# Kernel optimization log

Measured on AMD Instinct MI355X. Metric: run time of the kernel, lower is better.

The kernel has to match this reference:

```python
import jax, jax.numpy as jnp
import numpy as np

N = 100000      # nodes
E = 1600000     # edges (avg degree 16)
F_IN = 256      # num_features
H2 = 128        # nhid * 2 (layer 1 width)
H = 64          # nhid (layer 2 width)
C = 10          # num_classes


def setup_inputs() -> dict:
    key = jax.random.key(0)
    ks = jax.random.split(key, 8)
    x = jax.random.normal(ks[0], (N, F_IN), dtype=jnp.float32)
    edge_index = jax.random.randint(ks[1], (2, E), 0, N, dtype=jnp.int64)
    W1 = jax.random.normal(ks[2], (F_IN, H2), dtype=jnp.float32) / np.float32(np.sqrt(F_IN))
    b1 = jnp.zeros((H2,), jnp.float32)
    W2 = jax.random.normal(ks[3], (H2, H), dtype=jnp.float32) / np.float32(np.sqrt(H2))
    b2 = jnp.zeros((H,), jnp.float32)
    Wl = jax.random.normal(ks[4], (H, C), dtype=jnp.float32) / np.float32(np.sqrt(H))
    bl = jnp.zeros((C,), jnp.float32)
    return {"x": x, "edge_index": edge_index, "W1": W1, "b1": b1,
            "W2": W2, "b2": b2, "Wl": Wl, "bl": bl}


def reference(x, edge_index, W1, b1, W2, b2, Wl, bl):
    # --- GCN normalization with self-loops (PyG GCNConv default) ---
    loops = jnp.arange(N, dtype=edge_index.dtype)
    src = jnp.concatenate([edge_index[0], loops])  # message sources
    dst = jnp.concatenate([edge_index[1], loops])  # message targets
    deg = jax.ops.segment_sum(jnp.ones(src.shape[0], x.dtype), dst, num_segments=N)
    dinv = jnp.where(deg > 0, jax.lax.rsqrt(deg), 0.0)
    norm = dinv[src] * dinv[dst]                   # [E+N]

    def gcn_conv(h, W, b):
        m = h @ W                                  # transform first (out_channels small)
        agg = jax.ops.segment_sum(m[src] * norm[:, None], dst, num_segments=N)
        return agg + b

    h = jax.nn.relu(gcn_conv(x, W1, b1))           # [N, H2]
    h = jax.nn.relu(gcn_conv(h, W2, b2))           # [N, H]
    logits = h @ Wl + bl                            # [N, C]
    return jax.nn.log_softmax(logits, axis=-1)
```

## Files before the change

### kernel.cpp

```cpp
#include <hip/hip_runtime.h>


typedef unsigned short ushort_t;
typedef unsigned int uint_t;
typedef __attribute__((ext_vector_type(8))) short short8;
typedef __attribute__((ext_vector_type(4))) float floatx4;

static __device__ __forceinline__ ushort_t f2bf(float f) {
    union { float f; uint_t u; } c; c.f = f;
    return (ushort_t)((c.u + 0x8000u) >> 16);
}
static __device__ __forceinline__ float bf2f(ushort_t h) {
    union { uint_t u; float f; } c; c.u = ((uint_t)h) << 16;
    return c.f;
}
static __device__ __forceinline__ float2 up2(uint_t p) {
    union { uint_t u; float f; } lo, hi;
    lo.u = p << 16; hi.u = p & 0xffff0000u;
    return make_float2(lo.f, hi.f);
}
static __device__ __forceinline__ void ld_lds16(void* lds, const void* g) {
    __builtin_amdgcn_global_load_lds(
        (const __attribute__((address_space(1))) unsigned int*)g,
        (__attribute__((address_space(3))) unsigned int*)lds, 16, 0, 0);
}


__global__ __launch_bounds__(256) void deg_pos_kernel(
    const int* __restrict__ dst, int* __restrict__ cnt, int* __restrict__ pos, int E) {
    int i4 = (blockIdx.x * 256 + threadIdx.x) * 4;
    if (i4 + 3 < E) {
        int4 d = *(const int4*)(dst + i4);
        int4 p;
        p.x = atomicAdd(&cnt[d.x], 1);
        p.y = atomicAdd(&cnt[d.y], 1);
        p.z = atomicAdd(&cnt[d.z], 1);
        p.w = atomicAdd(&cnt[d.w], 1);
        *(int4*)(pos + i4) = p;
    } else {
        for (int e = i4; e < E; e++)
            pos[e] = atomicAdd(&cnt[dst[e]], 1);
    }
}

__global__ void scan_block(const int* __restrict__ cnt, int* __restrict__ rowptr,
                           int* __restrict__ bsums, float* __restrict__ dinv, int n) {
    __shared__ int s[256];
    int i = blockIdx.x * 256 + threadIdx.x;
    int v = (i < n) ? cnt[i] : 0;
    if (i < n) dinv[i] = rsqrtf((float)(v + 1));
    s[threadIdx.x] = v;
    __syncthreads();
    for (int off = 1; off < 256; off <<= 1) {
        int t = (threadIdx.x >= off) ? s[threadIdx.x - off] : 0;
        __syncthreads();
        s[threadIdx.x] += t;
        __syncthreads();
    }
    if (i < n) rowptr[i] = s[threadIdx.x] - v;
    if (threadIdx.x == 255) bsums[blockIdx.x] = s[255];
}

__global__ void scan_tops(const int* __restrict__ bsums, int* __restrict__ boffs, int nb) {
    __shared__ int s[512];
    int v = (threadIdx.x < nb) ? bsums[threadIdx.x] : 0;
    s[threadIdx.x] = v;
    __syncthreads();
    for (int off = 1; off < 512; off <<= 1) {
        int t = (threadIdx.x >= off) ? s[threadIdx.x - off] : 0;
        __syncthreads();
        s[threadIdx.x] += t;
        __syncthreads();
    }
    if (threadIdx.x < nb) boffs[threadIdx.x] = s[threadIdx.x] - v;
}

__global__ void finalize_rowptr(int* __restrict__ rowptr, const int* __restrict__ boffs,
                                int n, int E) {
    int i = blockIdx.x * 256 + threadIdx.x;
    if (i < n) rowptr[i] += boffs[blockIdx.x];
    if (i == 0) rowptr[n] = E;
}

__global__ __launch_bounds__(256) void place_kernel(
    const int* __restrict__ src, const int* __restrict__ dst,
    const int* __restrict__ pos, const int* __restrict__ rowptr,
    int* __restrict__ csr, int E) {
    int i4 = (blockIdx.x * 256 + threadIdx.x) * 4;
    if (i4 + 3 < E) {
        int4 s = *(const int4*)(src + i4);
        int4 d = *(const int4*)(dst + i4);
        int4 p = *(const int4*)(pos + i4);
        csr[rowptr[d.x] + p.x] = s.x;
        csr[rowptr[d.y] + p.y] = s.y;
        csr[rowptr[d.z] + p.z] = s.z;
        csr[rowptr[d.w] + p.w] = s.w;
    } else {
        for (int e = i4; e < E; e++)
            csr[rowptr[dst[e]] + pos[e]] = src[e];
    }
}

__global__ void wcvt2_kernel(const float* __restrict__ W1, const float* __restrict__ W2,
                             ushort_t* __restrict__ W1t, ushort_t* __restrict__ W2t) {
    int i = blockIdx.x * 256 + threadIdx.x;
    if (i < 256 * 128) {
        int k = i / 128, n = i % 128;
        W1t[n * 256 + k] = f2bf(W1[i]);
    }
    int j = i - 256 * 128;
    if (j >= 0 && j < 128 * 64) {
        int k = j / 64, n = j % 64;
        W2t[n * 128 + k] = f2bf(W2[j]);
    }
}

__global__ __launch_bounds__(256) void gemm1_mfma(
    const float* __restrict__ A, const ushort_t* __restrict__ Bt,
    const float* __restrict__ dinv, ushort_t* __restrict__ out, int M) {
    __shared__ float    As[2][128 * 32];
    __shared__ ushort_t Bs[2][128 * 32];
    const int tid = threadIdx.x;
    const int l = tid & 63;
    const int wave = tid >> 6;
    const int wm = wave >> 1, wn = wave & 1;
    const int lrow = l & 15, hh = l >> 4;
    const int m0 = blockIdx.x * 128;

    int aslot0[4], aslot1[4], bslot[4];
    #pragma unroll
    for (int mt = 0; mt < 4; mt++) {
        int r = wm * 64 + mt * 16 + lrow;
        int sw = r & 7;
        aslot0[mt] = (r * 8 + ((2 * hh) ^ sw)) * 4;
        aslot1[mt] = (r * 8 + ((2 * hh + 1) ^ sw)) * 4;
    }
    #pragma unroll
    for (int nt = 0; nt < 4; nt++) {
        int nc = wn * 64 + nt * 16 + lrow;
        bslot[nt] = (nc * 4 + (hh ^ ((nc >> 2) & 3))) * 8;
    }

    floatx4 acc[4][4];
    #pragma unroll
    for (int mt = 0; mt < 4; mt++)
        #pragma unroll
        for (int nt = 0; nt < 4; nt++)
            acc[mt][nt] = (floatx4){0.f, 0.f, 0.f, 0.f};

    auto stage = [&](int buf, int k0) {
        #pragma unroll
        for (int i = 0; i < 4; i++) {
            int s = i * 256 + tid;
            int r = s >> 3, cp = s & 7;
            int cg = cp ^ (r & 7);
            int row = m0 + r; if (row >= M) row = M - 1;
            ld_lds16(&As[buf][s * 4], A + (size_t)row * 256 + k0 + cg * 4);
        }
        #pragma unroll
        for (int i = 0; i < 2; i++) {
            int s = i * 256 + tid;
            int nn = s >> 2, cp = s & 3;
            int cg = cp ^ ((nn >> 2) & 3);
            ld_lds16(&Bs[buf][s * 8], Bt + (size_t)nn * 256 + k0 + cg * 8);
        }
    };

    stage(0, 0);
    __syncthreads();
    int buf = 0;
    for (int kk = 0; kk < 8; kk++) {
        if (kk < 7) stage(buf ^ 1, (kk + 1) * 32);
        short8 afr[4], bfr[4];
        #pragma unroll
        for (int mt = 0; mt < 4; mt++) {
            float4 u = *(const float4*)&As[buf][aslot0[mt]];
            float4 v = *(const float4*)&As[buf][aslot1[mt]];
            short8 t;
            t[0] = (short)f2bf(u.x); t[1] = (short)f2bf(u.y);
            t[2] = (short)f2bf(u.z); t[3] = (short)f2bf(u.w);
            t[4] = (short)f2bf(v.x); t[5] = (short)f2bf(v.y);
            t[6] = (short)f2bf(v.z); t[7] = (short)f2bf(v.w);
            afr[mt] = t;
        }
        #pragma unroll
        for (int nt = 0; nt < 4; nt++)
            bfr[nt] = *(const short8*)&Bs[buf][bslot[nt]];
        #pragma unroll
        for (int mt = 0; mt < 4; mt++)
            #pragma unroll
            for (int nt = 0; nt < 4; nt++)
                acc[mt][nt] = __builtin_amdgcn_mfma_f32_16x16x32_bf16(
                    afr[mt], bfr[nt], acc[mt][nt], 0, 0, 0);
        __syncthreads();
        buf ^= 1;
    }

    const int r0 = hh * 4;
    #pragma unroll
    for (int mt = 0; mt < 4; mt++) {
        int mbase = m0 + wm * 64 + mt * 16 + r0;
        float4 dv = *(const float4*)&dinv[mbase];
        float d[4] = {dv.x, dv.y, dv.z, dv.w};
        #pragma unroll
        for (int i = 0; i < 4; i++) {
            int m = mbase + i;
            if (m < M) {
                #pragma unroll
                for (int nt = 0; nt < 4; nt++)
                    out[(size_t)m * 128 + wn * 64 + nt * 16 + lrow] =
                        f2bf(acc[mt][nt][i] * d[i]);
            }
        }
    }
}

__global__ __launch_bounds__(256) void gemm2_mfma(
    const ushort_t* __restrict__ A, const ushort_t* __restrict__ Bt,
    const float* __restrict__ dinv, ushort_t* __restrict__ out, int M) {
    __shared__ ushort_t As[2][128 * 32];
    __shared__ ushort_t Bs[2][64 * 32];
    const int tid = threadIdx.x;
    const int l = tid & 63;
    const int wave = tid >> 6;
    const int wm = wave >> 1, wn = wave & 1;
    const int lrow = l & 15, hh = l >> 4;
    const int m0 = blockIdx.x * 128;

    int aslot[4], bslot[2];
    #pragma unroll
    for (int mt = 0; mt < 4; mt++) {
        int r = wm * 64 + mt * 16 + lrow;
        aslot[mt] = (r * 4 + (hh ^ ((r >> 2) & 3))) * 8;
    }
    #pragma unroll
    for (int nt = 0; nt < 2; nt++) {
        int nc = wn * 32 + nt * 16 + lrow;
        bslot[nt] = (nc * 4 + (hh ^ ((nc >> 2) & 3))) * 8;
    }

    floatx4 acc[4][2];
    #pragma unroll
    for (int mt = 0; mt < 4; mt++)
        #pragma unroll
        for (int nt = 0; nt < 2; nt++)
            acc[mt][nt] = (floatx4){0.f, 0.f, 0.f, 0.f};

    auto stage = [&](int buf, int k0) {
        #pragma unroll
        for (int i = 0; i < 2; i++) {
            int s = i * 256 + tid;
            int r = s >> 2, cp = s & 3;
            int cg = cp ^ ((r >> 2) & 3);
            int row = m0 + r; if (row >= M) row = M - 1;
            ld_lds16(&As[buf][s * 8], A + (size_t)row * 128 + k0 + cg * 8);
        }
        {
            int s = tid;
            int nn = s >> 2, cp = s & 3;
            int cg = cp ^ ((nn >> 2) & 3);
            ld_lds16(&Bs[buf][s * 8], Bt + (size_t)nn * 128 + k0 + cg * 8);
        }
    };

    stage(0, 0);
    __syncthreads();
    int buf = 0;
    for (int kk = 0; kk < 4; kk++) {
        if (kk < 3) stage(buf ^ 1, (kk + 1) * 32);
        short8 afr[4], bfr[2];
        #pragma unroll
        for (int mt = 0; mt < 4; mt++)
            afr[mt] = *(const short8*)&As[buf][aslot[mt]];
        #pragma unroll
        for (int nt = 0; nt < 2; nt++)
            bfr[nt] = *(const short8*)&Bs[buf][bslot[nt]];
        #pragma unroll
        for (int mt = 0; mt < 4; mt++)
            #pragma unroll
            for (int nt = 0; nt < 2; nt++)
                acc[mt][nt] = __builtin_amdgcn_mfma_f32_16x16x32_bf16(
                    afr[mt], bfr[nt], acc[mt][nt], 0, 0, 0);
        __syncthreads();
        buf ^= 1;
    }

    const int r0 = hh * 4;
    #pragma unroll
    for (int mt = 0; mt < 4; mt++) {
        int mbase = m0 + wm * 64 + mt * 16 + r0;
        float4 dv = *(const float4*)&dinv[mbase];
        float d[4] = {dv.x, dv.y, dv.z, dv.w};
        #pragma unroll
        for (int i = 0; i < 4; i++) {
            int m = mbase + i;
            if (m < M) {
                #pragma unroll
                for (int nt = 0; nt < 2; nt++)
                    out[(size_t)m * 64 + wn * 32 + nt * 16 + lrow] =
                        f2bf(acc[mt][nt][i] * d[i]);
            }
        }
    }
}

__global__ __launch_bounds__(256) void spmm_relu128(
    const ushort_t* __restrict__ Mm, const int* __restrict__ rowptr,
    const int* __restrict__ csr, const float* __restrict__ dinv,
    const float* __restrict__ bias, ushort_t* __restrict__ out, int n) {
    int v = (blockIdx.x * 256 + threadIdx.x) >> 6;
    int lane = threadIdx.x & 63;
    if (v >= n) return;
    int jb = rowptr[v], je = rowptr[v + 1];
    int cntn = je - jb;

    float2 accA = up2(*(const uint_t*)(Mm + (size_t)v * 128 + lane * 2));
    float2 accB = make_float2(0.f, 0.f);

    for (int base = 0; base < cntn; base += 64) {
        int m = cntn - base; if (m > 64) m = 64;
        int idx = (base + lane < cntn) ? csr[jb + base + lane] : 0;
        int jj = 0;
        for (; jj + 16 <= m; jj += 16) {
            int sI[16];
            #pragma unroll
            for (int t = 0; t < 16; t++) sI[t] = __shfl(idx, jj + t);
            uint_t p[16];
            #pragma unroll
            for (int t = 0; t < 16; t++)
                p[t] = *(const uint_t*)(Mm + (size_t)sI[t] * 128 + lane * 2);
            #pragma unroll
            for (int t = 0; t < 16; t++) {
                float2 f = up2(p[t]);
                if (t & 1) { accB.x += f.x; accB.y += f.y; }
                else       { accA.x += f.x; accA.y += f.y; }
            }
        }
        for (; jj + 8 <= m; jj += 8) {
            int sI[8];
            #pragma unroll
            for (int t = 0; t < 8; t++) sI[t] = __shfl(idx, jj + t);
            uint_t p[8];
            #pragma unroll
            for (int t = 0; t < 8; t++)
                p[t] = *(const uint_t*)(Mm + (size_t)sI[t] * 128 + lane * 2);
            #pragma unroll
            for (int t = 0; t < 8; t++) {
                float2 f = up2(p[t]);
                if (t & 1) { accB.x += f.x; accB.y += f.y; }
                else       { accA.x += f.x; accA.y += f.y; }
            }
        }
        for (; jj < m; jj++) {
            int s = __shfl(idx, jj);
            float2 f = up2(*(const uint_t*)(Mm + (size_t)s * 128 + lane * 2));
            accA.x += f.x; accA.y += f.y;
        }
    }
    float d = dinv[v];
    float2 bv = *(const float2*)&bias[lane * 2];
    float rx = fmaxf(d * (accA.x + accB.x) + bv.x, 0.f);
    float ry = fmaxf(d * (accA.y + accB.y) + bv.y, 0.f);
    uint_t packed = ((uint_t)f2bf(ry) << 16) | (uint_t)f2bf(rx);
    *(uint_t*)(out + (size_t)v * 128 + lane * 2) = packed;
}

__global__ __launch_bounds__(256) void spmm_relu64(
    const ushort_t* __restrict__ Mm, const int* __restrict__ rowptr,
    const int* __restrict__ csr, const float* __restrict__ dinv,
    const float* __restrict__ bias, ushort_t* __restrict__ out, int n) {
    int v = (blockIdx.x * 256 + threadIdx.x) >> 6;
    int lane = threadIdx.x & 63;
    if (v >= n) return;
    int jb = rowptr[v], je = rowptr[v + 1];
    int cntn = je - jb;

    float accA = bf2f(Mm[(size_t)v * 64 + lane]);
    float accB = 0.f;

    for (int base = 0; base < cntn; base += 64) {
        int m = cntn - base; if (m > 64) m = 64;
        int idx = (base + lane < cntn) ? csr[jb + base + lane] : 0;
        int jj = 0;
        for (; jj + 16 <= m; jj += 16) {
            int sI[16];
            #pragma unroll
            for (int t = 0; t < 16; t++) sI[t] = __shfl(idx, jj + t);
            ushort_t p[16];
            #pragma unroll
            for (int t = 0; t < 16; t++)
                p[t] = Mm[(size_t)sI[t] * 64 + lane];
            #pragma unroll
            for (int t = 0; t < 16; t++) {
                if (t & 1) accB += bf2f(p[t]);
                else       accA += bf2f(p[t]);
            }
        }
        for (; jj + 8 <= m; jj += 8) {
            int sI[8];
            #pragma unroll
            for (int t = 0; t < 8; t++) sI[t] = __shfl(idx, jj + t);
            ushort_t p[8];
            #pragma unroll
            for (int t = 0; t < 8; t++)
                p[t] = Mm[(size_t)sI[t] * 64 + lane];
            #pragma unroll
            for (int t = 0; t < 8; t++) {
                if (t & 1) accB += bf2f(p[t]);
                else       accA += bf2f(p[t]);
            }
        }
        for (; jj < m; jj++) {
            int s = __shfl(idx, jj);
            accA += bf2f(Mm[(size_t)s * 64 + lane]);
        }
    }
    float r = fmaxf(dinv[v] * (accA + accB) + bias[lane], 0.f);
    out[(size_t)v * 64 + lane] = f2bf(r);
}

__global__ __launch_bounds__(256) void head_kernel(
    const ushort_t* __restrict__ h2, const float* __restrict__ Wl,
    const float* __restrict__ bl, float* __restrict__ out, int n) {
    __shared__ float Ws[64 * 10];
    __shared__ float bs[10];
    for (int i = threadIdx.x; i < 640; i += 256) Ws[i] = Wl[i];
    if (threadIdx.x < 10) bs[threadIdx.x] = bl[threadIdx.x];
    __syncthreads();
    int v = blockIdx.x * 256 + threadIdx.x;
    if (v >= n) return;
    float acc[10];
    #pragma unroll
    for (int c = 0; c < 10; c++) acc[c] = bs[c];
    const ushort_t* hrow = &h2[(size_t)v * 64];
    #pragma unroll
    for (int k0 = 0; k0 < 64; k0 += 8) {
        short8 hv = *(const short8*)&hrow[k0];
        #pragma unroll
        for (int kk = 0; kk < 8; kk++) {
            float hf = bf2f((ushort_t)hv[kk]);
            #pragma unroll
            for (int c = 0; c < 10; c++)
                acc[c] += hf * Ws[(k0 + kk) * 10 + c];
        }
    }
    float m = acc[0];
    #pragma unroll
    for (int c = 1; c < 10; c++) m = fmaxf(m, acc[c]);
    float s = 0.f;
    #pragma unroll
    for (int c = 0; c < 10; c++) s += expf(acc[c] - m);
    float lse = logf(s);
    #pragma unroll
    for (int c = 0; c < 10; c++) out[(size_t)v * 10 + c] = acc[c] - m - lse;
}

extern "C" void kernel_launch(void* const* d_in, const int* in_sizes, int n_in,
                              void* d_out, int out_size, void* d_ws, size_t ws_size,
                              hipStream_t stream) {
    const float* x   = (const float*)d_in[0];
    const int*   ei  = (const int*)d_in[1];
    const float* W1  = (const float*)d_in[2];
    const float* b1  = (const float*)d_in[3];
    const float* W2  = (const float*)d_in[4];
    const float* b2  = (const float*)d_in[5];
    const float* Wl  = (const float*)d_in[6];
    const float* bl  = (const float*)d_in[7];
    float*       out = (float*)d_out;

    const int N = in_sizes[0] / 256;
    const int E = in_sizes[1] / 2;
    const int* srcI = ei;
    const int* dstI = ei + E;

    char* ws = (char*)d_ws;
    size_t off = 0;
    auto alloc = [&](size_t bytes) -> void* {
        void* p = ws + off;
        off = (off + bytes + 255) & ~(size_t)255;
        return p;
    };
    int*      cnt    = (int*)alloc((size_t)N * 4);
    int*      rowptr = (int*)alloc((size_t)(N + 1) * 4);
    float*    dinv   = (float*)alloc((size_t)(N + 128) * 4);
    int*      csr    = (int*)alloc((size_t)E * 4);
    int*      pos    = (int*)alloc((size_t)E * 4);
    int*      bsums  = (int*)alloc(512 * 4);
    int*      boffs  = (int*)alloc(512 * 4);
    ushort_t* W1t    = (ushort_t*)alloc((size_t)128 * 256 * 2);
    ushort_t* W2t    = (ushort_t*)alloc((size_t)64 * 128 * 2);
    ushort_t* bufA   = (ushort_t*)alloc((size_t)N * 128 * 2);
    ushort_t* bufB   = (ushort_t*)alloc((size_t)N * 128 * 2);

    hipMemsetAsync(cnt, 0, (size_t)N * 4, stream);

    const int nb = (N + 255) / 256;
    const int eb4 = (E + 1023) / 1024;
    deg_pos_kernel<<<eb4, 256, 0, stream>>>(dstI, cnt, pos, E);
    scan_block<<<nb, 256, 0, stream>>>(cnt, rowptr, bsums, dinv, N);
    scan_tops<<<1, 512, 0, stream>>>(bsums, boffs, nb);
    finalize_rowptr<<<nb, 256, 0, stream>>>(rowptr, boffs, N, E);
    place_kernel<<<eb4, 256, 0, stream>>>(srcI, dstI, pos, rowptr, csr, E);

    wcvt2_kernel<<<(256 * 128 + 128 * 64 + 255) / 256, 256, 0, stream>>>(W1, W2, W1t, W2t);

    const int gblk = (N + 127) / 128;
    gemm1_mfma<<<gblk, 256, 0, stream>>>(x, W1t, dinv, bufA, N);
    spmm_relu128<<<(N + 3) / 4, 256, 0, stream>>>(bufA, rowptr, csr, dinv, b1, bufB, N);
    gemm2_mfma<<<gblk, 256, 0, stream>>>(bufB, W2t, dinv, bufA, N);
    spmm_relu64<<<(N + 3) / 4, 256, 0, stream>>>(bufA, rowptr, csr, dinv, b2, bufB, N);
    head_kernel<<<(N + 255) / 256, 256, 0, stream>>>(bufB, Wl, bl, out, N);
}
```

Baseline: 436.8 us.

## Split degree counters into 8 privatized copies and use 32-bit byte offsets in SpMM

Degree counting now spreads atomics over eight counter arrays, picked by block index modulo 8, to cut contention. A new base_kernel computes per-copy starting offsets, and place_kernel uses those offsets to scatter CSR entries. Each thread now handles 8 edges instead of 4. The SpMM gathers precompute 32-bit byte offsets (row shifted plus lane offset) instead of 64-bit index multiplies, reducing address arithmetic. The cost is 8x larger counter and base buffers to zero and read, plus one extra kernel launch.

```diff
diff --git a/kernel.cpp b/kernel.cpp
--- a/kernel.cpp
+++ b/kernel.cpp
@@ -27,28 +27,41 @@
 
 
 __global__ __launch_bounds__(256) void deg_pos_kernel(
-    const int* __restrict__ dst, int* __restrict__ cnt, int* __restrict__ pos, int E) {
-    int i4 = (blockIdx.x * 256 + threadIdx.x) * 4;
-    if (i4 + 3 < E) {
-        int4 d = *(const int4*)(dst + i4);
-        int4 p;
-        p.x = atomicAdd(&cnt[d.x], 1);
-        p.y = atomicAdd(&cnt[d.y], 1);
-        p.z = atomicAdd(&cnt[d.z], 1);
-        p.w = atomicAdd(&cnt[d.w], 1);
-        *(int4*)(pos + i4) = p;
+    const int* __restrict__ dst, int* __restrict__ cnt8, int* __restrict__ pos,
+    int E, int N) {
+    int* cnt = cnt8 + (size_t)(blockIdx.x & 7) * N;
+    int i8 = (blockIdx.x * 256 + threadIdx.x) * 8;
+    if (i8 + 7 < E) {
+        int4 d0 = *(const int4*)(dst + i8);
+        int4 d1 = *(const int4*)(dst + i8 + 4);
+        int4 p0, p1;
+        p0.x = atomicAdd(&cnt[d0.x], 1);
+        p0.y = atomicAdd(&cnt[d0.y], 1);
+        p0.z = atomicAdd(&cnt[d0.z], 1);
+        p0.w = atomicAdd(&cnt[d0.w], 1);
+        p1.x = atomicAdd(&cnt[d1.x], 1);
+        p1.y = atomicAdd(&cnt[d1.y], 1);
+        p1.z = atomicAdd(&cnt[d1.z], 1);
+        p1.w = atomicAdd(&cnt[d1.w], 1);
+        *(int4*)(pos + i8) = p0;
+        *(int4*)(pos + i8 + 4) = p1;
     } else {
-        for (int e = i4; e < E; e++)
+        for (int e = i8; e < E; e++)
             pos[e] = atomicAdd(&cnt[dst[e]], 1);
     }
 }
 
-__global__ void scan_block(const int* __restrict__ cnt, int* __restrict__ rowptr,
-                           int* __restrict__ bsums, float* __restrict__ dinv, int n) {
+__global__ void scan_block(const int* __restrict__ cnt8, int* __restrict__ rowptr,
+                           int* __restrict__ bsums, float* __restrict__ dinv,
+                           int n, int N) {
     __shared__ int s[256];
     int i = blockIdx.x * 256 + threadIdx.x;
-    int v = (i < n) ? cnt[i] : 0;
-    if (i < n) dinv[i] = rsqrtf((float)(v + 1));
+    int v = 0;
+    if (i < n) {
+        #pragma unroll
+        for (int c = 0; c < 8; c++) v += cnt8[(size_t)c * N + i];
+        dinv[i] = rsqrtf((float)(v + 1));
+    }
     s[threadIdx.x] = v;
     __syncthreads();
     for (int off = 1; off < 256; off <<= 1) {
@@ -82,22 +95,43 @@
     if (i == 0) rowptr[n] = E;
 }
 
+__global__ void base_kernel(const int* __restrict__ cnt8, const int* __restrict__ rowptr,
+                            int* __restrict__ base8, int n, int N) {
+    int i = blockIdx.x * 256 + threadIdx.x;
+    if (i < n) {
+        int b = rowptr[i];
+        #pragma unroll
+        for (int c = 0; c < 8; c++) {
+            base8[(size_t)c * N + i] = b;
+            b += cnt8[(size_t)c * N + i];
+        }
+    }
+}
+
 __global__ __launch_bounds__(256) void place_kernel(
     const int* __restrict__ src, const int* __restrict__ dst,
-    const int* __restrict__ pos, const int* __restrict__ rowptr,
-    int* __restrict__ csr, int E) {
-    int i4 = (blockIdx.x * 256 + threadIdx.x) * 4;
-    if (i4 + 3 < E) {
-        int4 s = *(const int4*)(src + i4);
-        int4 d = *(const int4*)(dst + i4);
-        int4 p = *(const int4*)(pos + i4);
-        csr[rowptr[d.x] + p.x] = s.x;
-        csr[rowptr[d.y] + p.y] = s.y;
-        csr[rowptr[d.z] + p.z] = s.z;
-        csr[rowptr[d.w] + p.w] = s.w;
+    const int* __restrict__ pos, const int* __restrict__ base8,
+    int* __restrict__ csr, int E, int N) {
+    const int* base = base8 + (size_t)(blockIdx.x & 7) * N;
+    int i8 = (blockIdx.x * 256 + threadIdx.x) * 8;
+    if (i8 + 7 < E) {
+        int4 s0 = *(const int4*)(src + i8);
+        int4 s1 = *(const int4*)(src + i8 + 4);
+        int4 d0 = *(const int4*)(dst + i8);
+        int4 d1 = *(const int4*)(dst + i8 + 4);
+        int4 p0 = *(const int4*)(pos + i8);
+        int4 p1 = *(const int4*)(pos + i8 + 4);
+        csr[base[d0.x] + p0.x] = s0.x;
+        csr[base[d0.y] + p0.y] = s0.y;
+        csr[base[d0.z] + p0.z] = s0.z;
+        csr[base[d0.w] + p0.w] = s0.w;
+        csr[base[d1.x] + p1.x] = s1.x;
+        csr[base[d1.y] + p1.y] = s1.y;
+        csr[base[d1.z] + p1.z] = s1.z;
+        csr[base[d1.w] + p1.w] = s1.w;
     } else {
-        for (int e = i4; e < E; e++)
-            csr[rowptr[dst[e]] + pos[e]] = src[e];
+        for (int e = i8; e < E; e++)
+            csr[base[dst[e]] + pos[e]] = src[e];
     }
 }
 
@@ -313,22 +347,23 @@
     if (v >= n) return;
     int jb = rowptr[v], je = rowptr[v + 1];
     int cntn = je - jb;
-
-    float2 accA = up2(*(const uint_t*)(Mm + (size_t)v * 128 + lane * 2));
+    const char* Mb = (const char*)Mm;
+    const uint_t loff = lane * 4;
+
+    float2 accA = up2(*(const uint_t*)(Mb + ((size_t)v << 8) + loff));
     float2 accB = make_float2(0.f, 0.f);
 
     for (int base = 0; base < cntn; base += 64) {
         int m = cntn - base; if (m > 64) m = 64;
-        int idx = (base + lane < cntn) ? csr[jb + base + lane] : 0;
+        int roff = (base + lane < cntn) ? (csr[jb + base + lane] << 8) : 0;
         int jj = 0;
         for (; jj + 16 <= m; jj += 16) {
-            int sI[16];
-            #pragma unroll
-            for (int t = 0; t < 16; t++) sI[t] = __shfl(idx, jj + t);
+            uint_t o[16];
+            #pragma unroll
+            for (int t = 0; t < 16; t++) o[t] = (uint_t)__shfl(roff, jj + t) + loff;
             uint_t p[16];
             #pragma unroll
-            for (int t = 0; t < 16; t++)
-                p[t] = *(const uint_t*)(Mm + (size_t)sI[t] * 128 + lane * 2);
+            for (int t = 0; t < 16; t++) p[t] = *(const uint_t*)(Mb + o[t]);
             #pragma unroll
             for (int t = 0; t < 16; t++) {
                 float2 f = up2(p[t]);
@@ -337,13 +372,12 @@
             }
         }
         for (; jj + 8 <= m; jj += 8) {
-            int sI[8];
-            #pragma unroll
-            for (int t = 0; t < 8; t++) sI[t] = __shfl(idx, jj + t);
+            uint_t o[8];
+            #pragma unroll
+            for (int t = 0; t < 8; t++) o[t] = (uint_t)__shfl(roff, jj + t) + loff;
             uint_t p[8];
             #pragma unroll
-            for (int t = 0; t < 8; t++)
-                p[t] = *(const uint_t*)(Mm + (size_t)sI[t] * 128 + lane * 2);
+            for (int t = 0; t < 8; t++) p[t] = *(const uint_t*)(Mb + o[t]);
             #pragma unroll
             for (int t = 0; t < 8; t++) {
                 float2 f = up2(p[t]);
@@ -352,8 +386,8 @@
             }
         }
         for (; jj < m; jj++) {
-            int s = __shfl(idx, jj);
-            float2 f = up2(*(const uint_t*)(Mm + (size_t)s * 128 + lane * 2));
+            uint_t o = (uint_t)__shfl(roff, jj) + loff;
+            float2 f = up2(*(const uint_t*)(Mb + o));
             accA.x += f.x; accA.y += f.y;
         }
     }
@@ -374,22 +408,23 @@
     if (v >= n) return;
     int jb = rowptr[v], je = rowptr[v + 1];
     int cntn = je - jb;
-
-    float accA = bf2f(Mm[(size_t)v * 64 + lane]);
+    const char* Mb = (const char*)Mm;
+    const uint_t loff = lane * 2;
+
+    float accA = bf2f(*(const ushort_t*)(Mb + ((size_t)v << 7) + loff));
     float accB = 0.f;
 
     for (int base = 0; base < cntn; base += 64) {
         int m = cntn - base; if (m > 64) m = 64;
-        int idx = (base + lane < cntn) ? csr[jb + base + lane] : 0;
+        int roff = (base + lane < cntn) ? (csr[jb + base + lane] << 7) : 0;
         int jj = 0;
         for (; jj + 16 <= m; jj += 16) {
-            int sI[16];
-            #pragma unroll
-            for (int t = 0; t < 16; t++) sI[t] = __shfl(idx, jj + t);
+            uint_t o[16];
+            #pragma unroll
+            for (int t = 0; t < 16; t++) o[t] = (uint_t)__shfl(roff, jj + t) + loff;
             ushort_t p[16];
             #pragma unroll
-            for (int t = 0; t < 16; t++)
-                p[t] = Mm[(size_t)sI[t] * 64 + lane];
+            for (int t = 0; t < 16; t++) p[t] = *(const ushort_t*)(Mb + o[t]);
             #pragma unroll
             for (int t = 0; t < 16; t++) {
                 if (t & 1) accB += bf2f(p[t]);
@@ -397,13 +432,12 @@
             }
         }
         for (; jj + 8 <= m; jj += 8) {
-            int sI[8];
-            #pragma unroll
-            for (int t = 0; t < 8; t++) sI[t] = __shfl(idx, jj + t);
+            uint_t o[8];
+            #pragma unroll
+            for (int t = 0; t < 8; t++) o[t] = (uint_t)__shfl(roff, jj + t) + loff;
             ushort_t p[8];
             #pragma unroll
-            for (int t = 0; t < 8; t++)
-                p[t] = Mm[(size_t)sI[t] * 64 + lane];
+            for (int t = 0; t < 8; t++) p[t] = *(const ushort_t*)(Mb + o[t]);
             #pragma unroll
             for (int t = 0; t < 8; t++) {
                 if (t & 1) accB += bf2f(p[t]);
@@ -411,8 +445,8 @@
             }
         }
         for (; jj < m; jj++) {
-            int s = __shfl(idx, jj);
-            accA += bf2f(Mm[(size_t)s * 64 + lane]);
+            uint_t o = (uint_t)__shfl(roff, jj) + loff;
+            accA += bf2f(*(const ushort_t*)(Mb + o));
         }
     }
     float r = fmaxf(dinv[v] * (accA + accB) + bias[lane], 0.f);
@@ -480,7 +514,8 @@
         off = (off + bytes + 255) & ~(size_t)255;
         return p;
     };
-    int*      cnt    = (int*)alloc((size_t)N * 4);
+    int*      cnt8   = (int*)alloc((size_t)N * 8 * 4);
+    int*      base8  = (int*)alloc((size_t)N * 8 * 4);
     int*      rowptr = (int*)alloc((size_t)(N + 1) * 4);
     float*    dinv   = (float*)alloc((size_t)(N + 128) * 4);
     int*      csr    = (int*)alloc((size_t)E * 4);
@@ -492,15 +527,16 @@
     ushort_t* bufA   = (ushort_t*)alloc((size_t)N * 128 * 2);
     ushort_t* bufB   = (ushort_t*)alloc((size_t)N * 128 * 2);
 
-    hipMemsetAsync(cnt, 0, (size_t)N * 4, stream);
+    hipMemsetAsync(cnt8, 0, (size_t)N * 8 * 4, stream);
 
     const int nb = (N + 255) / 256;
-    const int eb4 = (E + 1023) / 1024;
-    deg_pos_kernel<<<eb4, 256, 0, stream>>>(dstI, cnt, pos, E);
-    scan_block<<<nb, 256, 0, stream>>>(cnt, rowptr, bsums, dinv, N);
+    const int eb8 = (E + 2047) / 2048;
+    deg_pos_kernel<<<eb8, 256, 0, stream>>>(dstI, cnt8, pos, E, N);
+    scan_block<<<nb, 256, 0, stream>>>(cnt8, rowptr, bsums, dinv, N, N);
     scan_tops<<<1, 512, 0, stream>>>(bsums, boffs, nb);
     finalize_rowptr<<<nb, 256, 0, stream>>>(rowptr, boffs, N, E);
-    place_kernel<<<eb4, 256, 0, stream>>>(srcI, dstI, pos, rowptr, csr, E);
+    base_kernel<<<nb, 256, 0, stream>>>(cnt8, rowptr, base8, N, N);
+    place_kernel<<<eb8, 256, 0, stream>>>(srcI, dstI, pos, base8, csr, E, N);
 
     wcvt2_kernel<<<(256 * 128 + 128 * 64 + 255) / 256, 256, 0, stream>>>(W1, W2, W1t, W2t);
 
```

Result: no change. 429.0 us (-1.8%).
